# Kernel optimization log

Hardware: AMD Instinct MI355X
Metric: run time of the kernel (lower is better)

The kernel has to match this reference:

```python
import jax, jax.numpy as jnp
import numpy as np

B = 2048        # graphs per batch
NC = 81         # cells per sudoku
IN_C, HID = 10, 128
N_ACT, N_NUM, N_TECH = 4, 9, 10


def _sudoku_edges():
    idx = np.arange(NC).reshape(9, 9)
    adj = np.zeros((NC, NC), dtype=bool)
    for i in range(9):
        for j in range(9):
            n = idx[i, j]
            adj[n, idx[i, :]] = True
            adj[n, idx[:, j]] = True
            bi, bj = 3 * (i // 3), 3 * (j // 3)
            adj[n, idx[bi:bi + 3, bj:bj + 3].reshape(-1)] = True
            adj[n, n] = False
    src, dst = np.nonzero(adj)  # 1620 directed edges
    return np.stack([src, dst]).astype(np.int32)


def setup_inputs() -> dict:
    key = jax.random.key(0)
    ks = jax.random.split(key, 12)
    N = B * NC
    base = _sudoku_edges()                          # [2, 1620]
    offs = (np.arange(B, dtype=np.int32) * NC)      # [B]
    ei = (base[:, None, :] + offs[None, :, None]).reshape(2, -1)  # [2, B*1620]
    batch = np.repeat(np.arange(B, dtype=np.int32), NC)           # [N]

    def lin(k, fan_in, fan_out):
        s = 1.0 / np.sqrt(fan_in)
        return jax.random.uniform(k, (fan_in, fan_out), jnp.float32, -s, s)

    return {
        "x": jax.random.normal(ks[0], (N, IN_C), jnp.float32),
        "edge_index": jnp.asarray(ei),
        "batch": jnp.asarray(batch),
        "W1": lin(ks[1], IN_C, HID), "b1": jnp.zeros((HID,), jnp.float32),
        "W2": lin(ks[2], HID, HID),  "b2": jnp.zeros((HID,), jnp.float32),
        "Wa": lin(ks[3], HID, N_ACT),  "ba": jnp.zeros((N_ACT,), jnp.float32),
        "Wc": lin(ks[4], HID, NC),     "bc": jnp.zeros((NC,), jnp.float32),
        "Wn": lin(ks[5], HID, N_NUM),  "bn": jnp.zeros((N_NUM,), jnp.float32),
        "Wt": lin(ks[6], HID, N_TECH), "bt": jnp.zeros((N_TECH,), jnp.float32),
    }


def _gcn_conv(x, edge_index, W, b):
    n = x.shape[0]
    loop = jnp.arange(n, dtype=edge_index.dtype)
    src = jnp.concatenate([edge_index[0], loop])
    dst = jnp.concatenate([edge_index[1], loop])
    deg = jax.ops.segment_sum(jnp.ones_like(dst, jnp.float32), dst, num_segments=n)
    dinv = jax.lax.rsqrt(deg)            # deg >= 1 due to self-loops
    norm = dinv[src] * dinv[dst]         # [E+N]
    h = x @ W                            # [N, out]
    msg = h[src] * norm[:, None]         # gather + scale
    return jax.ops.segment_sum(msg, dst, num_segments=n) + b


def reference(x, edge_index, batch, W1, b1, W2, b2, Wa, ba, Wc, bc, Wn, bn, Wt, bt):
    h = jax.nn.relu(_gcn_conv(x, edge_index, W1, b1))
    h = jax.nn.relu(_gcn_conv(h, edge_index, W2, b2))
    # global mean pool over graphs
    sums = jax.ops.segment_sum(h, batch, num_segments=B)
    cnts = jax.ops.segment_sum(jnp.ones((h.shape[0],), h.dtype), batch, num_segments=B)
    pooled = sums / jnp.maximum(cnts, 1.0)[:, None]   # [B, HID]
    return (pooled @ Wa + ba, pooled @ Wc + bc, pooled @ Wn + bn, pooled @ Wt + bt)
```

## Files before the change

kernel.cpp:

```cpp
#include <hip/hip_runtime.h>
#include <hip/hip_bf16.h>

typedef __attribute__((ext_vector_type(8))) short bf16x8;
typedef __attribute__((ext_vector_type(4))) float f32x4;

__device__ __forceinline__ unsigned short f2b(float f) {
    __hip_bfloat16 h = __float2bfloat16(f);
    return __builtin_bit_cast(unsigned short, h);
}
__device__ __forceinline__ float b2f(unsigned short u) {
    unsigned v = ((unsigned)u) << 16;
    return __builtin_bit_cast(float, v);
}
__device__ __forceinline__ float ldf(const void* p, int idx, bool f32) {
    return f32 ? ((const float*)p)[idx] : b2f(((const unsigned short*)p)[idx]);
}
__device__ __forceinline__ unsigned short ldb(const void* p, int idx, bool f32) {
    return f32 ? f2b(((const float*)p)[idx]) : ((const unsigned short*)p)[idx];
}
__device__ __forceinline__ int swz(int row, int col) {
    return row * 128 + (((col >> 3) ^ (row & 7)) << 3) + (col & 7);
}

__device__ __forceinline__ bool sniff_f32(const void* x) {
    const unsigned* p = (const unsigned*)x;
    int wild = 0;
#pragma unroll
    for (int i = 0; i < 16; ++i) {
        unsigned e = (p[i] >> 7) & 0xFF;
        wild += (e != 0 && (e < 0x68 || e > 0x90)) ? 1 : 0;
    }
    return wild > 8;
}

#define WS_B1F    16
#define WS_B2F    528
#define WS_BHF    1040
#define WS_W1R    1536
#define WS_W2R    9728
#define WS_SR     42496
#define WS_WH     60928

__global__ void k_repack(const void* __restrict__ x,
                         const void* __restrict__ W1, const void* __restrict__ b1,
                         const void* __restrict__ W2, const void* __restrict__ b2,
                         const void* __restrict__ Wa, const void* __restrict__ ba,
                         const void* __restrict__ Wc, const void* __restrict__ bc,
                         const void* __restrict__ Wn, const void* __restrict__ bn,
                         const void* __restrict__ Wt, const void* __restrict__ bt,
                         char* __restrict__ ws) {
    const bool f32 = sniff_f32(x);
    int idx = blockIdx.x * blockDim.x + threadIdx.x;
    if (idx < 4096) {
        int f = idx >> 5, k = idx & 31;
        unsigned short v = (k < 10) ? ldb(W1, k * 128 + f, f32) : (unsigned short)0;
        ((unsigned short*)(ws + WS_W1R))[idx] = v;
        return;
    }
    idx -= 4096;
    if (idx < 16384) {
        int f = idx >> 7, k = idx & 127;
        ((unsigned short*)(ws + WS_W2R))[idx] = ldb(W2, k * 128 + f, f32);
        return;
    }
    idx -= 16384;
    if (idx < 9216) {
        int fi = idx >> 9, rem = idx & 511;
        int lane = rem >> 3, j = rem & 7;
        int mi = fi / 3, kc = fi - mi * 3;
        int node = mi * 16 + (lane & 15);
        int cell = kc * 32 + ((lane >> 4) << 3) + j;
        bool adj = false;
        if (node < 81 && cell < 81) {
            int ni = node / 9, nj = node % 9;
            int ci = cell / 9, cj = cell % 9;
            adj = (ni == ci) || (nj == cj) ||
                  ((ni / 3 == ci / 3) && (nj / 3 == cj / 3));
        }
        ((unsigned short*)(ws + WS_SR))[idx] = adj ? (unsigned short)0x3F80 : (unsigned short)0;
        return;
    }
    idx -= 9216;
    if (idx < 13312) {
        int o = idx >> 7, f = idx & 127;
        const void* W; int oo, dim;
        if (o < 4)       { W = Wa; oo = o;      dim = 4;  }
        else if (o < 85) { W = Wc; oo = o - 4;  dim = 81; }
        else if (o < 94) { W = Wn; oo = o - 85; dim = 9;  }
        else             { W = Wt; oo = o - 94; dim = 10; }
        ((float*)(ws + WS_WH))[idx] = ldf(W, f * dim + oo, f32);
        return;
    }
    idx -= 13312;
    if (idx < 360) {
        float v;
        if (idx < 128)      v = ldf(b1, idx, f32);
        else if (idx < 256) v = ldf(b2, idx - 128, f32);
        else {
            int o = idx - 256;
            if (o < 4)       v = ldf(ba, o, f32);
            else if (o < 85) v = ldf(bc, o - 4, f32);
            else if (o < 94) v = ldf(bn, o - 85, f32);
            else             v = ldf(bt, o - 94, f32);
        }
        if (idx < 128)      ((float*)(ws + WS_B1F))[idx] = v;
        else if (idx < 256) ((float*)(ws + WS_B2F))[idx - 128] = v;
        else                ((float*)(ws + WS_BHF))[idx - 256] = v;
    }
}

__global__ __launch_bounds__(256, 2) void sudoku_gnn(
    const void* __restrict__ x, const char* __restrict__ ws,
    void* __restrict__ out, int nB)
{
    __shared__ __attribute__((aligned(16))) unsigned short sA[16384];
    __shared__ __attribute__((aligned(16))) unsigned short sB[16384];
    __shared__ __attribute__((aligned(16))) unsigned int   xs2[1632];
    __shared__ float sPoolPart[2][256];
    __shared__ float sPool[2][128];

    const bool f32 = sniff_f32(x);
    const unsigned short* w1r = (const unsigned short*)(ws + WS_W1R);
    const unsigned short* w2r = (const unsigned short*)(ws + WS_W2R);
    const unsigned short* sr  = (const unsigned short*)(ws + WS_SR);
    const float* b1f = (const float*)(ws + WS_B1F);
    const float* b2f = (const float*)(ws + WS_B2F);
    const float* bhf = (const float*)(ws + WS_BHF);
    const float* whf = (const float*)(ws + WS_WH);

    const int tid  = threadIdx.x;
    const int wave = tid >> 6;
    const int lane = tid & 63;
    const int ln15 = lane & 15;
    const int q    = lane >> 4;
    const int k0   = q * 8;
    const int mtb  = (wave & 1) * 3;
    const int nb   = (wave & 1) * 48;
    const int fb   = (wave >> 1) * 64;
    const int g0   = blockIdx.x * 2;
    const int g1   = g0 + 1;
    const bool hasB = (g1 < nB);
    const float inv21 = 1.0f / 21.0f;
    unsigned short* const buf[2] = {sA, sB};

    {
        const int words = f32 ? 810 : 405;
        const int tot = words * (hasB ? 2 : 1);
        const unsigned int* src = (const unsigned int*)x + (size_t)g0 * words;
        for (int i = tid; i < tot; i += 256) xs2[i] = src[i];
    }

    bf16x8 sfr[3][3];
#pragma unroll
    for (int kc = 0; kc < 3; ++kc)
#pragma unroll
        for (int jt = 0; jt < 3; ++jt)
            sfr[kc][jt] = *(const bf16x8*)&sr[(((mtb + jt) * 3 + kc) * 64 + lane) * 8];
    bf16x8 w1f[4];
#pragma unroll
    for (int nt = 0; nt < 4; ++nt)
        w1f[nt] = *(const bf16x8*)&w1r[(fb + nt * 16 + ln15) * 32 + k0];

    __syncthreads();

    bf16x8 xf[2][3];
#pragma unroll
    for (int gg = 0; gg < 2; ++gg)
#pragma unroll
        for (int mt = 0; mt < 3; ++mt) {
            int node = (mtb + mt) * 16 + ln15;
            bf16x8 v = {0, 0, 0, 0, 0, 0, 0, 0};
            if (node < 81) {
                int base = gg * 810 + node * 10;
                if (q == 0) {
#pragma unroll
                    for (int jj = 0; jj < 8; ++jj)
                        v[jj] = (short)(f32 ? f2b(((const float*)xs2)[base + jj])
                                            : ((const unsigned short*)xs2)[base + jj]);
                } else if (q == 1) {
#pragma unroll
                    for (int jj = 0; jj < 2; ++jj)
                        v[jj] = (short)(f32 ? f2b(((const float*)xs2)[base + 8 + jj])
                                            : ((const unsigned short*)xs2)[base + 8 + jj]);
                }
            }
            xf[gg][mt] = v;
        }

    const f32x4 z4 = {0.f, 0.f, 0.f, 0.f};
    f32x4 acc[2][3][4];

#pragma unroll
    for (int gg = 0; gg < 2; ++gg)
#pragma unroll
        for (int mt = 0; mt < 3; ++mt)
#pragma unroll
            for (int nt = 0; nt < 4; ++nt)
                acc[gg][mt][nt] = __builtin_amdgcn_mfma_f32_16x16x32_bf16(xf[gg][mt], w1f[nt], z4, 0, 0, 0);
#pragma unroll
    for (int gg = 0; gg < 2; ++gg)
#pragma unroll
        for (int mt = 0; mt < 3; ++mt)
#pragma unroll
            for (int nt = 0; nt < 4; ++nt) {
                int f = fb + nt * 16 + ln15;
                int nodeb = (mtb + mt) * 16 + q * 4;
                unsigned lo = (unsigned)f2b(acc[gg][mt][nt][0]) | ((unsigned)f2b(acc[gg][mt][nt][1]) << 16);
                unsigned hi = (unsigned)f2b(acc[gg][mt][nt][2]) | ((unsigned)f2b(acc[gg][mt][nt][3]) << 16);
                *(uint2*)&buf[gg][swz(f, nodeb)] = make_uint2(lo, hi);
            }
    __syncthreads();

#pragma unroll
    for (int gg = 0; gg < 2; ++gg)
#pragma unroll
        for (int a = 0; a < 3; ++a)
#pragma unroll
            for (int b = 0; b < 4; ++b) acc[gg][a][b] = z4;
#pragma unroll
    for (int kc = 0; kc < 3; ++kc) {
        bf16x8 a4[2][4];
#pragma unroll
        for (int gg = 0; gg < 2; ++gg)
#pragma unroll
            for (int at = 0; at < 4; ++at)
                a4[gg][at] = *(const bf16x8*)&buf[gg][swz(fb + at * 16 + ln15, kc * 32 + k0)];
#pragma unroll
        for (int gg = 0; gg < 2; ++gg)
#pragma unroll
            for (int at = 0; at < 4; ++at)
#pragma unroll
                for (int jt = 0; jt < 3; ++jt)
                    acc[gg][jt][at] = __builtin_amdgcn_mfma_f32_16x16x32_bf16(a4[gg][at], sfr[kc][jt], acc[gg][jt][at], 0, 0, 0);
    }
    __syncthreads();
#pragma unroll
    for (int gg = 0; gg < 2; ++gg)
#pragma unroll
        for (int at = 0; at < 4; ++at) {
            float4 bv = *(const float4*)&b1f[fb + at * 16 + q * 4];
#pragma unroll
            for (int jt = 0; jt < 3; ++jt) {
                int node = nb + jt * 16 + ln15;
                float v0 = fmaxf(acc[gg][jt][at][0] * inv21 + bv.x, 0.0f);
                float v1 = fmaxf(acc[gg][jt][at][1] * inv21 + bv.y, 0.0f);
                float v2 = fmaxf(acc[gg][jt][at][2] * inv21 + bv.z, 0.0f);
                float v3 = fmaxf(acc[gg][jt][at][3] * inv21 + bv.w, 0.0f);
                unsigned lo = (unsigned)f2b(v0) | ((unsigned)f2b(v1) << 16);
                unsigned hi = (unsigned)f2b(v2) | ((unsigned)f2b(v3) << 16);
                *(uint2*)&buf[gg][swz(node, fb + at * 16 + q * 4)] = make_uint2(lo, hi);
            }
        }
    __syncthreads();

#pragma unroll
    for (int gg = 0; gg < 2; ++gg)
#pragma unroll
        for (int a = 0; a < 3; ++a)
#pragma unroll
            for (int b = 0; b < 4; ++b) acc[gg][a][b] = z4;
#pragma unroll
    for (int kc = 0; kc < 4; ++kc) {
        bf16x8 w2f[4];
#pragma unroll
        for (int nt = 0; nt < 4; ++nt)
            w2f[nt] = *(const bf16x8*)&w2r[(fb + nt * 16 + ln15) * 128 + kc * 32 + k0];
        bf16x8 a3[2][3];
#pragma unroll
        for (int gg = 0; gg < 2; ++gg)
#pragma unroll
            for (int mt = 0; mt < 3; ++mt)
                a3[gg][mt] = *(const bf16x8*)&buf[gg][swz((mtb + mt) * 16 + ln15, kc * 32 + k0)];
#pragma unroll
        for (int gg = 0; gg < 2; ++gg)
#pragma unroll
            for (int mt = 0; mt < 3; ++mt)
#pragma unroll
                for (int nt = 0; nt < 4; ++nt)
                    acc[gg][mt][nt] = __builtin_amdgcn_mfma_f32_16x16x32_bf16(a3[gg][mt], w2f[nt], acc[gg][mt][nt], 0, 0, 0);
    }
    __syncthreads();
#pragma unroll
    for (int gg = 0; gg < 2; ++gg)
#pragma unroll
        for (int mt = 0; mt < 3; ++mt)
#pragma unroll
            for (int nt = 0; nt < 4; ++nt) {
                int f = fb + nt * 16 + ln15;
                int nodeb = (mtb + mt) * 16 + q * 4;
                unsigned lo = (unsigned)f2b(acc[gg][mt][nt][0]) | ((unsigned)f2b(acc[gg][mt][nt][1]) << 16);
                unsigned hi = (unsigned)f2b(acc[gg][mt][nt][2]) | ((unsigned)f2b(acc[gg][mt][nt][3]) << 16);
                *(uint2*)&buf[gg][swz(f, nodeb)] = make_uint2(lo, hi);
            }
    __syncthreads();

#pragma unroll
    for (int gg = 0; gg < 2; ++gg)
#pragma unroll
        for (int a = 0; a < 3; ++a)
#pragma unroll
            for (int b = 0; b < 4; ++b) acc[gg][a][b] = z4;
#pragma unroll
    for (int kc = 0; kc < 3; ++kc) {
        bf16x8 a4[2][4];
#pragma unroll
        for (int gg = 0; gg < 2; ++gg)
#pragma unroll
            for (int at = 0; at < 4; ++at)
                a4[gg][at] = *(const bf16x8*)&buf[gg][swz(fb + at * 16 + ln15, kc * 32 + k0)];
#pragma unroll
        for (int gg = 0; gg < 2; ++gg)
#pragma unroll
            for (int at = 0; at < 4; ++at)
#pragma unroll
                for (int jt = 0; jt < 3; ++jt)
                    acc[gg][jt][at] = __builtin_amdgcn_mfma_f32_16x16x32_bf16(a4[gg][at], sfr[kc][jt], acc[gg][jt][at], 0, 0, 0);
    }
#pragma unroll
    for (int gg = 0; gg < 2; ++gg)
#pragma unroll
        for (int at = 0; at < 4; ++at) {
            float4 bv = *(const float4*)&b2f[fb + at * 16 + q * 4];
            float s0 = 0.f, s1 = 0.f, s2 = 0.f, s3 = 0.f;
#pragma unroll
            for (int jt = 0; jt < 3; ++jt) {
                int node = nb + jt * 16 + ln15;
                if (node < 81) {
                    s0 += fmaxf(acc[gg][jt][at][0] * inv21 + bv.x, 0.0f);
                    s1 += fmaxf(acc[gg][jt][at][1] * inv21 + bv.y, 0.0f);
                    s2 += fmaxf(acc[gg][jt][at][2] * inv21 + bv.z, 0.0f);
                    s3 += fmaxf(acc[gg][jt][at][3] * inv21 + bv.w, 0.0f);
                }
            }
#pragma unroll
            for (int off = 1; off < 16; off <<= 1) {
                s0 += __shfl_xor(s0, off);
                s1 += __shfl_xor(s1, off);
                s2 += __shfl_xor(s2, off);
                s3 += __shfl_xor(s3, off);
            }
            if (ln15 == 0) {
                float4 v = {s0, s1, s2, s3};
                *(float4*)&sPoolPart[gg][(wave & 1) * 128 + fb + at * 16 + q * 4] = v;
            }
        }
    __syncthreads();
    {
        int gg = tid >> 7;
        int f  = tid & 127;
        sPool[gg][f] = (sPoolPart[gg][f] + sPoolPart[gg][128 + f]) / 81.0f;
    }
    __syncthreads();

    {
        int gg = tid >> 7;
        int o  = tid & 127;
        int g  = gg ? g1 : g0;
        if (o < 104 && (gg == 0 || hasB)) {
            float a = bhf[o];
            const float4* wrow = (const float4*)(whf + o * 128);
            const float4* sp4  = (const float4*)sPool[gg];
#pragma unroll 8
            for (int i = 0; i < 32; ++i) {
                float4 wv = wrow[i];
                float4 pv = sp4[i];
                a += pv.x * wv.x + pv.y * wv.y + pv.z * wv.z + pv.w * wv.w;
            }
            int oo; size_t off;
            if (o < 4)       { oo = o;      off = (size_t)g * 4 + oo; }
            else if (o < 85) { oo = o - 4;  off = (size_t)nB * 4  + (size_t)g * 81 + oo; }
            else if (o < 94) { oo = o - 85; off = (size_t)nB * 85 + (size_t)g * 9  + oo; }
            else             { oo = o - 94; off = (size_t)nB * 94 + (size_t)g * 10 + oo; }
            if (f32) ((float*)out)[off] = a;
            else     ((unsigned short*)out)[off] = f2b(a);
        }
    }
}

extern "C" void kernel_launch(void* const* d_in, const int* in_sizes, int n_in,
                              void* d_out, int out_size, void* d_ws, size_t ws_size,
                              hipStream_t stream) {
    const void* x  = d_in[0];
    int nB = in_sizes[2] / 81;
    if (nB <= 0) return;

    char* ws = (char*)d_ws;
    hipLaunchKernelGGL(k_repack, dim3(170), dim3(256), 0, stream,
                       x, d_in[3], d_in[4], d_in[5], d_in[6],
                       d_in[7], d_in[8], d_in[9], d_in[10],
                       d_in[11], d_in[12], d_in[13], d_in[14], ws);
    hipLaunchKernelGGL(sudoku_gnn, dim3((nB + 1) / 2), dim3(256), 0, stream,
                       x, (const char*)ws, d_out, nB);
}
```

Measured before the change: 144.4 us.

## Fold both GCN layers into one loop with padded-stride LDS layout

Replaces the XOR-swizzled LDS buffers with padded row strides (136 and 104 shorts) in one shared array, and loads x directly into LDS as bf16 rows instead of staging raw words. The two GCN layers share a rolled loop with rolled k-chunk loops, which shrinks code size and likely register pressure. LDS usage drops, which may help occupancy. In exchange the rolled loops can limit instruction scheduling and MFMA/load overlap, and padding may leave some bank conflicts.

```diff
diff --git a/kernel.cpp b/kernel.cpp
--- a/kernel.cpp
+++ b/kernel.cpp
@@ -17,9 +17,6 @@
 }
 __device__ __forceinline__ unsigned short ldb(const void* p, int idx, bool f32) {
     return f32 ? f2b(((const float*)p)[idx]) : ((const unsigned short*)p)[idx];
-}
-__device__ __forceinline__ int swz(int row, int col) {
-    return row * 128 + (((col >> 3) ^ (row & 7)) << 3) + (col & 7);
 }
 
 __device__ __forceinline__ bool sniff_f32(const void* x) {
@@ -109,13 +106,14 @@
     }
 }
 
+#define TS 104
+#define HS 136
+
 __global__ __launch_bounds__(256, 2) void sudoku_gnn(
     const void* __restrict__ x, const char* __restrict__ ws,
     void* __restrict__ out, int nB)
 {
-    __shared__ __attribute__((aligned(16))) unsigned short sA[16384];
-    __shared__ __attribute__((aligned(16))) unsigned short sB[16384];
-    __shared__ __attribute__((aligned(16))) unsigned int   xs2[1632];
+    __shared__ __attribute__((aligned(16))) unsigned short sG[2][13312];
     __shared__ float sPoolPart[2][256];
     __shared__ float sPool[2][128];
 
@@ -138,17 +136,9 @@
     const int nb   = (wave & 1) * 48;
     const int fb   = (wave >> 1) * 64;
     const int g0   = blockIdx.x * 2;
-    const int g1   = g0 + 1;
-    const bool hasB = (g1 < nB);
+    const bool hasB = (g0 + 1 < nB);
+    const int g1   = hasB ? (g0 + 1) : g0;
     const float inv21 = 1.0f / 21.0f;
-    unsigned short* const buf[2] = {sA, sB};
-
-    {
-        const int words = f32 ? 810 : 405;
-        const int tot = words * (hasB ? 2 : 1);
-        const unsigned int* src = (const unsigned int*)x + (size_t)g0 * words;
-        for (int i = tid; i < tot; i += 256) xs2[i] = src[i];
-    }
 
     bf16x8 sfr[3][3];
 #pragma unroll
@@ -156,206 +146,179 @@
 #pragma unroll
         for (int jt = 0; jt < 3; ++jt)
             sfr[kc][jt] = *(const bf16x8*)&sr[(((mtb + jt) * 3 + kc) * 64 + lane) * 8];
-    bf16x8 w1f[4];
-#pragma unroll
-    for (int nt = 0; nt < 4; ++nt)
-        w1f[nt] = *(const bf16x8*)&w1r[(fb + nt * 16 + ln15) * 32 + k0];
-
+
+#pragma unroll 1
+    for (int idx = tid; idx < 96 * 16 * 2; idx += 256) {
+        int gg  = idx >= 96 * 16;
+        int r   = idx - gg * 96 * 16;
+        int row = r >> 4, col = (r & 15) * 2;
+        int g   = gg ? g1 : g0;
+        unsigned short v0 = 0, v1 = 0;
+        if (row < 81) {
+            int base = (g * 81 + row) * 10;
+            if (col < 10)     v0 = ldb(x, base + col, f32);
+            if (col + 1 < 10) v1 = ldb(x, base + col + 1, f32);
+        }
+        *(unsigned*)&sG[gg][row * HS + col] = (unsigned)v0 | ((unsigned)v1 << 16);
+    }
     __syncthreads();
-
-    bf16x8 xf[2][3];
-#pragma unroll
-    for (int gg = 0; gg < 2; ++gg)
-#pragma unroll
-        for (int mt = 0; mt < 3; ++mt) {
-            int node = (mtb + mt) * 16 + ln15;
-            bf16x8 v = {0, 0, 0, 0, 0, 0, 0, 0};
-            if (node < 81) {
-                int base = gg * 810 + node * 10;
-                if (q == 0) {
-#pragma unroll
-                    for (int jj = 0; jj < 8; ++jj)
-                        v[jj] = (short)(f32 ? f2b(((const float*)xs2)[base + jj])
-                                            : ((const unsigned short*)xs2)[base + jj]);
-                } else if (q == 1) {
-#pragma unroll
-                    for (int jj = 0; jj < 2; ++jj)
-                        v[jj] = (short)(f32 ? f2b(((const float*)xs2)[base + 8 + jj])
-                                            : ((const unsigned short*)xs2)[base + 8 + jj]);
-                }
-            }
-            xf[gg][mt] = v;
-        }
 
     const f32x4 z4 = {0.f, 0.f, 0.f, 0.f};
     f32x4 acc[2][3][4];
 
-#pragma unroll
-    for (int gg = 0; gg < 2; ++gg)
-#pragma unroll
-        for (int mt = 0; mt < 3; ++mt)
+#pragma unroll 1
+    for (int l = 0; l < 2; ++l) {
+        const unsigned short* w = l ? w2r : w1r;
+        const int ldw = l ? 128 : 32;
+        const int kcn = l ? 4 : 1;
+
+        {
+            bf16x8 wf[4], a3[2][3];
 #pragma unroll
             for (int nt = 0; nt < 4; ++nt)
-                acc[gg][mt][nt] = __builtin_amdgcn_mfma_f32_16x16x32_bf16(xf[gg][mt], w1f[nt], z4, 0, 0, 0);
-#pragma unroll
-    for (int gg = 0; gg < 2; ++gg)
-#pragma unroll
-        for (int mt = 0; mt < 3; ++mt)
-#pragma unroll
-            for (int nt = 0; nt < 4; ++nt) {
-                int f = fb + nt * 16 + ln15;
-                int nodeb = (mtb + mt) * 16 + q * 4;
-                unsigned lo = (unsigned)f2b(acc[gg][mt][nt][0]) | ((unsigned)f2b(acc[gg][mt][nt][1]) << 16);
-                unsigned hi = (unsigned)f2b(acc[gg][mt][nt][2]) | ((unsigned)f2b(acc[gg][mt][nt][3]) << 16);
-                *(uint2*)&buf[gg][swz(f, nodeb)] = make_uint2(lo, hi);
+                wf[nt] = *(const bf16x8*)&w[(fb + nt * 16 + ln15) * ldw + k0];
+#pragma unroll
+            for (int gg = 0; gg < 2; ++gg)
+#pragma unroll
+                for (int mt = 0; mt < 3; ++mt)
+                    a3[gg][mt] = *(const bf16x8*)&sG[gg][((mtb + mt) * 16 + ln15) * HS + k0];
+#pragma unroll
+            for (int gg = 0; gg < 2; ++gg)
+#pragma unroll
+                for (int mt = 0; mt < 3; ++mt)
+#pragma unroll
+                    for (int nt = 0; nt < 4; ++nt)
+                        acc[gg][mt][nt] = __builtin_amdgcn_mfma_f32_16x16x32_bf16(a3[gg][mt], wf[nt], z4, 0, 0, 0);
+        }
+#pragma unroll 1
+        for (int kc = 1; kc < kcn; ++kc) {
+            bf16x8 wf[4], a3[2][3];
+#pragma unroll
+            for (int nt = 0; nt < 4; ++nt)
+                wf[nt] = *(const bf16x8*)&w[(fb + nt * 16 + ln15) * ldw + kc * 32 + k0];
+#pragma unroll
+            for (int gg = 0; gg < 2; ++gg)
+#pragma unroll
+                for (int mt = 0; mt < 3; ++mt)
+                    a3[gg][mt] = *(const bf16x8*)&sG[gg][((mtb + mt) * 16 + ln15) * HS + kc * 32 + k0];
+#pragma unroll
+            for (int gg = 0; gg < 2; ++gg)
+#pragma unroll
+                for (int mt = 0; mt < 3; ++mt)
+#pragma unroll
+                    for (int nt = 0; nt < 4; ++nt)
+                        acc[gg][mt][nt] = __builtin_amdgcn_mfma_f32_16x16x32_bf16(a3[gg][mt], wf[nt], acc[gg][mt][nt], 0, 0, 0);
+        }
+        __syncthreads();
+
+#pragma unroll
+        for (int gg = 0; gg < 2; ++gg)
+#pragma unroll
+            for (int mt = 0; mt < 3; ++mt)
+#pragma unroll
+                for (int nt = 0; nt < 4; ++nt) {
+                    int f = fb + nt * 16 + ln15;
+                    int cellb = (mtb + mt) * 16 + q * 4;
+                    unsigned lo = (unsigned)f2b(acc[gg][mt][nt][0]) | ((unsigned)f2b(acc[gg][mt][nt][1]) << 16);
+                    unsigned hi = (unsigned)f2b(acc[gg][mt][nt][2]) | ((unsigned)f2b(acc[gg][mt][nt][3]) << 16);
+                    *(uint2*)&sG[gg][f * TS + cellb] = make_uint2(lo, hi);
+                }
+        __syncthreads();
+
+        {
+            bf16x8 a4[2][4];
+#pragma unroll
+            for (int gg = 0; gg < 2; ++gg)
+#pragma unroll
+                for (int at = 0; at < 4; ++at)
+                    a4[gg][at] = *(const bf16x8*)&sG[gg][(fb + at * 16 + ln15) * TS + k0];
+#pragma unroll
+            for (int gg = 0; gg < 2; ++gg)
+#pragma unroll
+                for (int at = 0; at < 4; ++at)
+#pragma unroll
+                    for (int jt = 0; jt < 3; ++jt)
+                        acc[gg][jt][at] = __builtin_amdgcn_mfma_f32_16x16x32_bf16(a4[gg][at], sfr[0][jt], z4, 0, 0, 0);
+        }
+#pragma unroll 1
+        for (int kc = 1; kc < 3; ++kc) {
+            bf16x8 a4[2][4];
+#pragma unroll
+            for (int gg = 0; gg < 2; ++gg)
+#pragma unroll
+                for (int at = 0; at < 4; ++at)
+                    a4[gg][at] = *(const bf16x8*)&sG[gg][(fb + at * 16 + ln15) * TS + kc * 32 + k0];
+#pragma unroll
+            for (int gg = 0; gg < 2; ++gg)
+#pragma unroll
+                for (int at = 0; at < 4; ++at)
+#pragma unroll
+                    for (int jt = 0; jt < 3; ++jt)
+                        acc[gg][jt][at] = __builtin_amdgcn_mfma_f32_16x16x32_bf16(a4[gg][at], sfr[kc][jt], acc[gg][jt][at], 0, 0, 0);
+        }
+        __syncthreads();
+
+        if (l == 0) {
+#pragma unroll
+            for (int gg = 0; gg < 2; ++gg)
+#pragma unroll
+                for (int at = 0; at < 4; ++at) {
+                    float4 bv = *(const float4*)&b1f[fb + at * 16 + q * 4];
+#pragma unroll
+                    for (int jt = 0; jt < 3; ++jt) {
+                        int node = nb + jt * 16 + ln15;
+                        float v0 = fmaxf(acc[gg][jt][at][0] * inv21 + bv.x, 0.0f);
+                        float v1 = fmaxf(acc[gg][jt][at][1] * inv21 + bv.y, 0.0f);
+                        float v2 = fmaxf(acc[gg][jt][at][2] * inv21 + bv.z, 0.0f);
+                        float v3 = fmaxf(acc[gg][jt][at][3] * inv21 + bv.w, 0.0f);
+                        unsigned lo = (unsigned)f2b(v0) | ((unsigned)f2b(v1) << 16);
+                        unsigned hi = (unsigned)f2b(v2) | ((unsigned)f2b(v3) << 16);
+                        *(uint2*)&sG[gg][node * HS + fb + at * 16 + q * 4] = make_uint2(lo, hi);
+                    }
+                }
+            __syncthreads();
+        } else {
+#pragma unroll
+            for (int gg = 0; gg < 2; ++gg)
+#pragma unroll
+                for (int at = 0; at < 4; ++at) {
+                    float4 bv = *(const float4*)&b2f[fb + at * 16 + q * 4];
+                    float s0 = 0.f, s1 = 0.f, s2 = 0.f, s3 = 0.f;
+#pragma unroll
+                    for (int jt = 0; jt < 3; ++jt) {
+                        int node = nb + jt * 16 + ln15;
+                        if (node < 81) {
+                            s0 += fmaxf(acc[gg][jt][at][0] * inv21 + bv.x, 0.0f);
+                            s1 += fmaxf(acc[gg][jt][at][1] * inv21 + bv.y, 0.0f);
+                            s2 += fmaxf(acc[gg][jt][at][2] * inv21 + bv.z, 0.0f);
+                            s3 += fmaxf(acc[gg][jt][at][3] * inv21 + bv.w, 0.0f);
+                        }
+                    }
+#pragma unroll
+                    for (int off = 1; off < 16; off <<= 1) {
+                        s0 += __shfl_xor(s0, off);
+                        s1 += __shfl_xor(s1, off);
+                        s2 += __shfl_xor(s2, off);
+                        s3 += __shfl_xor(s3, off);
+                    }
+                    if (ln15 == 0) {
+                        float4 v = {s0, s1, s2, s3};
+                        *(float4*)&sPoolPart[gg][(wave & 1) * 128 + fb + at * 16 + q * 4] = v;
+                    }
+                }
+            __syncthreads();
+            {
+                int gg = tid >> 7, f = tid & 127;
+                sPool[gg][f] = (sPoolPart[gg][f] + sPoolPart[gg][128 + f]) * (1.0f / 81.0f);
             }
-    __syncthreads();
-
-#pragma unroll
-    for (int gg = 0; gg < 2; ++gg)
-#pragma unroll
-        for (int a = 0; a < 3; ++a)
-#pragma unroll
-            for (int b = 0; b < 4; ++b) acc[gg][a][b] = z4;
-#pragma unroll
-    for (int kc = 0; kc < 3; ++kc) {
-        bf16x8 a4[2][4];
-#pragma unroll
-        for (int gg = 0; gg < 2; ++gg)
-#pragma unroll
-            for (int at = 0; at < 4; ++at)
-                a4[gg][at] = *(const bf16x8*)&buf[gg][swz(fb + at * 16 + ln15, kc * 32 + k0)];
-#pragma unroll
-        for (int gg = 0; gg < 2; ++gg)
-#pragma unroll
-            for (int at = 0; at < 4; ++at)
-#pragma unroll
-                for (int jt = 0; jt < 3; ++jt)
-                    acc[gg][jt][at] = __builtin_amdgcn_mfma_f32_16x16x32_bf16(a4[gg][at], sfr[kc][jt], acc[gg][jt][at], 0, 0, 0);
-    }
-    __syncthreads();
-#pragma unroll
-    for (int gg = 0; gg < 2; ++gg)
-#pragma unroll
-        for (int at = 0; at < 4; ++at) {
-            float4 bv = *(const float4*)&b1f[fb + at * 16 + q * 4];
-#pragma unroll
-            for (int jt = 0; jt < 3; ++jt) {
-                int node = nb + jt * 16 + ln15;
-                float v0 = fmaxf(acc[gg][jt][at][0] * inv21 + bv.x, 0.0f);
-                float v1 = fmaxf(acc[gg][jt][at][1] * inv21 + bv.y, 0.0f);
-                float v2 = fmaxf(acc[gg][jt][at][2] * inv21 + bv.z, 0.0f);
-                float v3 = fmaxf(acc[gg][jt][at][3] * inv21 + bv.w, 0.0f);
-                unsigned lo = (unsigned)f2b(v0) | ((unsigned)f2b(v1) << 16);
-                unsigned hi = (unsigned)f2b(v2) | ((unsigned)f2b(v3) << 16);
-                *(uint2*)&buf[gg][swz(node, fb + at * 16 + q * 4)] = make_uint2(lo, hi);
-            }
-        }
-    __syncthreads();
-
-#pragma unroll
-    for (int gg = 0; gg < 2; ++gg)
-#pragma unroll
-        for (int a = 0; a < 3; ++a)
-#pragma unroll
-            for (int b = 0; b < 4; ++b) acc[gg][a][b] = z4;
-#pragma unroll
-    for (int kc = 0; kc < 4; ++kc) {
-        bf16x8 w2f[4];
-#pragma unroll
-        for (int nt = 0; nt < 4; ++nt)
-            w2f[nt] = *(const bf16x8*)&w2r[(fb + nt * 16 + ln15) * 128 + kc * 32 + k0];
-        bf16x8 a3[2][3];
-#pragma unroll
-        for (int gg = 0; gg < 2; ++gg)
-#pragma unroll
-            for (int mt = 0; mt < 3; ++mt)
-                a3[gg][mt] = *(const bf16x8*)&buf[gg][swz((mtb + mt) * 16 + ln15, kc * 32 + k0)];
-#pragma unroll
-        for (int gg = 0; gg < 2; ++gg)
-#pragma unroll
-            for (int mt = 0; mt < 3; ++mt)
-#pragma unroll
-                for (int nt = 0; nt < 4; ++nt)
-                    acc[gg][mt][nt] = __builtin_amdgcn_mfma_f32_16x16x32_bf16(a3[gg][mt], w2f[nt], acc[gg][mt][nt], 0, 0, 0);
-    }
-    __syncthreads();
-#pragma unroll
-    for (int gg = 0; gg < 2; ++gg)
-#pragma unroll
-        for (int mt = 0; mt < 3; ++mt)
-#pragma unroll
-            for (int nt = 0; nt < 4; ++nt) {
-                int f = fb + nt * 16 + ln15;
-                int nodeb = (mtb + mt) * 16 + q * 4;
-                unsigned lo = (unsigned)f2b(acc[gg][mt][nt][0]) | ((unsigned)f2b(acc[gg][mt][nt][1]) << 16);
-                unsigned hi = (unsigned)f2b(acc[gg][mt][nt][2]) | ((unsigned)f2b(acc[gg][mt][nt][3]) << 16);
-                *(uint2*)&buf[gg][swz(f, nodeb)] = make_uint2(lo, hi);
-            }
-    __syncthreads();
-
-#pragma unroll
-    for (int gg = 0; gg < 2; ++gg)
-#pragma unroll
-        for (int a = 0; a < 3; ++a)
-#pragma unroll
-            for (int b = 0; b < 4; ++b) acc[gg][a][b] = z4;
-#pragma unroll
-    for (int kc = 0; kc < 3; ++kc) {
-        bf16x8 a4[2][4];
-#pragma unroll
-        for (int gg = 0; gg < 2; ++gg)
-#pragma unroll
-            for (int at = 0; at < 4; ++at)
-                a4[gg][at] = *(const bf16x8*)&buf[gg][swz(fb + at * 16 + ln15, kc * 32 + k0)];
-#pragma unroll
-        for (int gg = 0; gg < 2; ++gg)
-#pragma unroll
-            for (int at = 0; at < 4; ++at)
-#pragma unroll
-                for (int jt = 0; jt < 3; ++jt)
-                    acc[gg][jt][at] = __builtin_amdgcn_mfma_f32_16x16x32_bf16(a4[gg][at], sfr[kc][jt], acc[gg][jt][at], 0, 0, 0);
-    }
-#pragma unroll
-    for (int gg = 0; gg < 2; ++gg)
-#pragma unroll
-        for (int at = 0; at < 4; ++at) {
-            float4 bv = *(const float4*)&b2f[fb + at * 16 + q * 4];
-            float s0 = 0.f, s1 = 0.f, s2 = 0.f, s3 = 0.f;
-#pragma unroll
-            for (int jt = 0; jt < 3; ++jt) {
-                int node = nb + jt * 16 + ln15;
-                if (node < 81) {
-                    s0 += fmaxf(acc[gg][jt][at][0] * inv21 + bv.x, 0.0f);
-                    s1 += fmaxf(acc[gg][jt][at][1] * inv21 + bv.y, 0.0f);
-                    s2 += fmaxf(acc[gg][jt][at][2] * inv21 + bv.z, 0.0f);
-                    s3 += fmaxf(acc[gg][jt][at][3] * inv21 + bv.w, 0.0f);
-                }
-            }
-#pragma unroll
-            for (int off = 1; off < 16; off <<= 1) {
-                s0 += __shfl_xor(s0, off);
-                s1 += __shfl_xor(s1, off);
-                s2 += __shfl_xor(s2, off);
-                s3 += __shfl_xor(s3, off);
-            }
-            if (ln15 == 0) {
-                float4 v = {s0, s1, s2, s3};
-                *(float4*)&sPoolPart[gg][(wave & 1) * 128 + fb + at * 16 + q * 4] = v;
-            }
-        }
-    __syncthreads();
-    {
-        int gg = tid >> 7;
-        int f  = tid & 127;
-        sPool[gg][f] = (sPoolPart[gg][f] + sPoolPart[gg][128 + f]) / 81.0f;
-    }
-    __syncthreads();
+            __syncthreads();
+        }
+    }
 
     {
         int gg = tid >> 7;
         int o  = tid & 127;
-        int g  = gg ? g1 : g0;
+        int g  = gg ? (g0 + 1) : g0;
         if (o < 104 && (gg == 0 || hasB)) {
             float a = bhf[o];
             const float4* wrow = (const float4*)(whf + o * 128);
```

Measured after the change: 161.8 us. 1.12x slower.

## Fold normalization scales into weights, shrink LDS with padded layout, load x directly

Applied to the files above, without the earlier changes.

Folds the 1/21 GCN normalization into W1/W2 and the 1/81 mean-pool factor into the head weights during repack, which removes per-element multiplies from the epilogues. Replaces the two 32KB swizzled LDS buffers, the staged x copy and the separate pool arrays with one padded buffer (row strides 104/136) that is reused for pooling partials. This lowers LDS use and may allow more resident blocks. Also reads x straight from global memory, caches the dtype sniff result in the workspace, uses a manual RNE bf16 pack, and seeds the first MFMA with zero instead of clearing accumulators. In exchange, folding the scale before bf16 rounding changes numerics slightly, and the padded strides may cause more LDS bank conflicts than the swizzle did.

```diff
diff --git a/kernel.cpp b/kernel.cpp
--- a/kernel.cpp
+++ b/kernel.cpp
@@ -18,10 +18,13 @@
 __device__ __forceinline__ unsigned short ldb(const void* p, int idx, bool f32) {
     return f32 ? f2b(((const float*)p)[idx]) : ((const unsigned short*)p)[idx];
 }
-__device__ __forceinline__ int swz(int row, int col) {
-    return row * 128 + (((col >> 3) ^ (row & 7)) << 3) + (col & 7);
-}
-
+__device__ __forceinline__ unsigned packRNE(float x, float y) {
+    unsigned a = __builtin_bit_cast(unsigned, x);
+    unsigned b = __builtin_bit_cast(unsigned, y);
+    a += 0x7fffu + ((a >> 16) & 1u);
+    b += 0x7fffu + ((b >> 16) & 1u);
+    return (a >> 16) | (b & 0xffff0000u);
+}
 __device__ __forceinline__ bool sniff_f32(const void* x) {
     const unsigned* p = (const unsigned*)x;
     int wild = 0;
@@ -33,6 +36,7 @@
     return wild > 8;
 }
 
+#define WS_FLAG   0
 #define WS_B1F    16
 #define WS_B2F    528
 #define WS_BHF    1040
@@ -50,17 +54,19 @@
                          const void* __restrict__ Wt, const void* __restrict__ bt,
                          char* __restrict__ ws) {
     const bool f32 = sniff_f32(x);
+    const float inv21 = 1.0f / 21.0f;
+    if (blockIdx.x == 0 && threadIdx.x == 0) *(int*)(ws + WS_FLAG) = f32 ? 1 : 0;
     int idx = blockIdx.x * blockDim.x + threadIdx.x;
     if (idx < 4096) {
         int f = idx >> 5, k = idx & 31;
-        unsigned short v = (k < 10) ? ldb(W1, k * 128 + f, f32) : (unsigned short)0;
+        unsigned short v = (k < 10) ? f2b(ldf(W1, k * 128 + f, f32) * inv21) : (unsigned short)0;
         ((unsigned short*)(ws + WS_W1R))[idx] = v;
         return;
     }
     idx -= 4096;
     if (idx < 16384) {
         int f = idx >> 7, k = idx & 127;
-        ((unsigned short*)(ws + WS_W2R))[idx] = ldb(W2, k * 128 + f, f32);
+        ((unsigned short*)(ws + WS_W2R))[idx] = f2b(ldf(W2, k * 128 + f, f32) * inv21);
         return;
     }
     idx -= 16384;
@@ -88,7 +94,7 @@
         else if (o < 85) { W = Wc; oo = o - 4;  dim = 81; }
         else if (o < 94) { W = Wn; oo = o - 85; dim = 9;  }
         else             { W = Wt; oo = o - 94; dim = 10; }
-        ((float*)(ws + WS_WH))[idx] = ldf(W, f * dim + oo, f32);
+        ((float*)(ws + WS_WH))[idx] = ldf(W, f * dim + oo, f32) * (1.0f / 81.0f);
         return;
     }
     idx -= 13312;
@@ -109,17 +115,16 @@
     }
 }
 
+#define TS 104
+#define HS 136
+
 __global__ __launch_bounds__(256, 2) void sudoku_gnn(
     const void* __restrict__ x, const char* __restrict__ ws,
     void* __restrict__ out, int nB)
 {
-    __shared__ __attribute__((aligned(16))) unsigned short sA[16384];
-    __shared__ __attribute__((aligned(16))) unsigned short sB[16384];
-    __shared__ __attribute__((aligned(16))) unsigned int   xs2[1632];
-    __shared__ float sPoolPart[2][256];
-    __shared__ float sPool[2][128];
-
-    const bool f32 = sniff_f32(x);
+    __shared__ __attribute__((aligned(16))) unsigned short sG[2][13312];
+
+    const bool f32 = (*(const int*)(ws + WS_FLAG)) != 0;
     const unsigned short* w1r = (const unsigned short*)(ws + WS_W1R);
     const unsigned short* w2r = (const unsigned short*)(ws + WS_W2R);
     const unsigned short* sr  = (const unsigned short*)(ws + WS_SR);
@@ -138,17 +143,8 @@
     const int nb   = (wave & 1) * 48;
     const int fb   = (wave >> 1) * 64;
     const int g0   = blockIdx.x * 2;
-    const int g1   = g0 + 1;
-    const bool hasB = (g1 < nB);
-    const float inv21 = 1.0f / 21.0f;
-    unsigned short* const buf[2] = {sA, sB};
-
-    {
-        const int words = f32 ? 810 : 405;
-        const int tot = words * (hasB ? 2 : 1);
-        const unsigned int* src = (const unsigned int*)x + (size_t)g0 * words;
-        for (int i = tid; i < tot; i += 256) xs2[i] = src[i];
-    }
+    const bool hasB = (g0 + 1 < nB);
+    const int g1   = hasB ? (g0 + 1) : g0;
 
     bf16x8 sfr[3][3];
 #pragma unroll
@@ -161,27 +157,22 @@
     for (int nt = 0; nt < 4; ++nt)
         w1f[nt] = *(const bf16x8*)&w1r[(fb + nt * 16 + ln15) * 32 + k0];
 
-    __syncthreads();
-
     bf16x8 xf[2][3];
 #pragma unroll
     for (int gg = 0; gg < 2; ++gg)
 #pragma unroll
         for (int mt = 0; mt < 3; ++mt) {
             int node = (mtb + mt) * 16 + ln15;
+            int g = gg ? g1 : g0;
             bf16x8 v = {0, 0, 0, 0, 0, 0, 0, 0};
             if (node < 81) {
-                int base = gg * 810 + node * 10;
+                int base = (g * 81 + node) * 10;
                 if (q == 0) {
 #pragma unroll
-                    for (int jj = 0; jj < 8; ++jj)
-                        v[jj] = (short)(f32 ? f2b(((const float*)xs2)[base + jj])
-                                            : ((const unsigned short*)xs2)[base + jj]);
+                    for (int jj = 0; jj < 8; ++jj) v[jj] = (short)ldb(x, base + jj, f32);
                 } else if (q == 1) {
-#pragma unroll
-                    for (int jj = 0; jj < 2; ++jj)
-                        v[jj] = (short)(f32 ? f2b(((const float*)xs2)[base + 8 + jj])
-                                            : ((const unsigned short*)xs2)[base + 8 + jj]);
+                    v[0] = (short)ldb(x, base + 8, f32);
+                    v[1] = (short)ldb(x, base + 9, f32);
                 }
             }
             xf[gg][mt] = v;
@@ -204,36 +195,41 @@
 #pragma unroll
             for (int nt = 0; nt < 4; ++nt) {
                 int f = fb + nt * 16 + ln15;
-                int nodeb = (mtb + mt) * 16 + q * 4;
-                unsigned lo = (unsigned)f2b(acc[gg][mt][nt][0]) | ((unsigned)f2b(acc[gg][mt][nt][1]) << 16);
-                unsigned hi = (unsigned)f2b(acc[gg][mt][nt][2]) | ((unsigned)f2b(acc[gg][mt][nt][3]) << 16);
-                *(uint2*)&buf[gg][swz(f, nodeb)] = make_uint2(lo, hi);
-            }
-    __syncthreads();
-
-#pragma unroll
-    for (int gg = 0; gg < 2; ++gg)
-#pragma unroll
-        for (int a = 0; a < 3; ++a)
-#pragma unroll
-            for (int b = 0; b < 4; ++b) acc[gg][a][b] = z4;
+                int cellb = (mtb + mt) * 16 + q * 4;
+                *(uint2*)&sG[gg][f * TS + cellb] =
+                    make_uint2(packRNE(acc[gg][mt][nt][0], acc[gg][mt][nt][1]),
+                               packRNE(acc[gg][mt][nt][2], acc[gg][mt][nt][3]));
+            }
+    __syncthreads();
+
 #pragma unroll
     for (int kc = 0; kc < 3; ++kc) {
-        bf16x8 a4[2][4];
+        bf16x8 afr[2][4];
 #pragma unroll
         for (int gg = 0; gg < 2; ++gg)
 #pragma unroll
             for (int at = 0; at < 4; ++at)
-                a4[gg][at] = *(const bf16x8*)&buf[gg][swz(fb + at * 16 + ln15, kc * 32 + k0)];
-#pragma unroll
-        for (int gg = 0; gg < 2; ++gg)
-#pragma unroll
-            for (int at = 0; at < 4; ++at)
-#pragma unroll
-                for (int jt = 0; jt < 3; ++jt)
-                    acc[gg][jt][at] = __builtin_amdgcn_mfma_f32_16x16x32_bf16(a4[gg][at], sfr[kc][jt], acc[gg][jt][at], 0, 0, 0);
-    }
-    __syncthreads();
+                afr[gg][at] = *(const bf16x8*)&sG[gg][(fb + at * 16 + ln15) * TS + kc * 32 + k0];
+        if (kc == 0) {
+#pragma unroll
+            for (int gg = 0; gg < 2; ++gg)
+#pragma unroll
+                for (int at = 0; at < 4; ++at)
+#pragma unroll
+                    for (int jt = 0; jt < 3; ++jt)
+                        acc[gg][jt][at] = __builtin_amdgcn_mfma_f32_16x16x32_bf16(afr[gg][at], sfr[0][jt], z4, 0, 0, 0);
+        } else {
+#pragma unroll
+            for (int gg = 0; gg < 2; ++gg)
+#pragma unroll
+                for (int at = 0; at < 4; ++at)
+#pragma unroll
+                    for (int jt = 0; jt < 3; ++jt)
+                        acc[gg][jt][at] = __builtin_amdgcn_mfma_f32_16x16x32_bf16(afr[gg][at], sfr[kc][jt], acc[gg][jt][at], 0, 0, 0);
+        }
+    }
+    __syncthreads();
+
 #pragma unroll
     for (int gg = 0; gg < 2; ++gg)
 #pragma unroll
@@ -242,44 +238,47 @@
 #pragma unroll
             for (int jt = 0; jt < 3; ++jt) {
                 int node = nb + jt * 16 + ln15;
-                float v0 = fmaxf(acc[gg][jt][at][0] * inv21 + bv.x, 0.0f);
-                float v1 = fmaxf(acc[gg][jt][at][1] * inv21 + bv.y, 0.0f);
-                float v2 = fmaxf(acc[gg][jt][at][2] * inv21 + bv.z, 0.0f);
-                float v3 = fmaxf(acc[gg][jt][at][3] * inv21 + bv.w, 0.0f);
-                unsigned lo = (unsigned)f2b(v0) | ((unsigned)f2b(v1) << 16);
-                unsigned hi = (unsigned)f2b(v2) | ((unsigned)f2b(v3) << 16);
-                *(uint2*)&buf[gg][swz(node, fb + at * 16 + q * 4)] = make_uint2(lo, hi);
-            }
-        }
-    __syncthreads();
-
-#pragma unroll
-    for (int gg = 0; gg < 2; ++gg)
-#pragma unroll
-        for (int a = 0; a < 3; ++a)
-#pragma unroll
-            for (int b = 0; b < 4; ++b) acc[gg][a][b] = z4;
+                float v0 = fmaxf(acc[gg][jt][at][0] + bv.x, 0.0f);
+                float v1 = fmaxf(acc[gg][jt][at][1] + bv.y, 0.0f);
+                float v2 = fmaxf(acc[gg][jt][at][2] + bv.z, 0.0f);
+                float v3 = fmaxf(acc[gg][jt][at][3] + bv.w, 0.0f);
+                *(uint2*)&sG[gg][node * HS + fb + at * 16 + q * 4] =
+                    make_uint2(packRNE(v0, v1), packRNE(v2, v3));
+            }
+        }
+    __syncthreads();
+
 #pragma unroll
     for (int kc = 0; kc < 4; ++kc) {
-        bf16x8 w2f[4];
+        bf16x8 w2f[4], a3[2][3];
 #pragma unroll
         for (int nt = 0; nt < 4; ++nt)
             w2f[nt] = *(const bf16x8*)&w2r[(fb + nt * 16 + ln15) * 128 + kc * 32 + k0];
-        bf16x8 a3[2][3];
 #pragma unroll
         for (int gg = 0; gg < 2; ++gg)
 #pragma unroll
             for (int mt = 0; mt < 3; ++mt)
-                a3[gg][mt] = *(const bf16x8*)&buf[gg][swz((mtb + mt) * 16 + ln15, kc * 32 + k0)];
-#pragma unroll
-        for (int gg = 0; gg < 2; ++gg)
-#pragma unroll
-            for (int mt = 0; mt < 3; ++mt)
-#pragma unroll
-                for (int nt = 0; nt < 4; ++nt)
-                    acc[gg][mt][nt] = __builtin_amdgcn_mfma_f32_16x16x32_bf16(a3[gg][mt], w2f[nt], acc[gg][mt][nt], 0, 0, 0);
-    }
-    __syncthreads();
+                a3[gg][mt] = *(const bf16x8*)&sG[gg][((mtb + mt) * 16 + ln15) * HS + kc * 32 + k0];
+        if (kc == 0) {
+#pragma unroll
+            for (int gg = 0; gg < 2; ++gg)
+#pragma unroll
+                for (int mt = 0; mt < 3; ++mt)
+#pragma unroll
+                    for (int nt = 0; nt < 4; ++nt)
+                        acc[gg][mt][nt] = __builtin_amdgcn_mfma_f32_16x16x32_bf16(a3[gg][mt], w2f[nt], z4, 0, 0, 0);
+        } else {
+#pragma unroll
+            for (int gg = 0; gg < 2; ++gg)
+#pragma unroll
+                for (int mt = 0; mt < 3; ++mt)
+#pragma unroll
+                    for (int nt = 0; nt < 4; ++nt)
+                        acc[gg][mt][nt] = __builtin_amdgcn_mfma_f32_16x16x32_bf16(a3[gg][mt], w2f[nt], acc[gg][mt][nt], 0, 0, 0);
+        }
+    }
+    __syncthreads();
+
 #pragma unroll
     for (int gg = 0; gg < 2; ++gg)
 #pragma unroll
@@ -287,35 +286,40 @@
 #pragma unroll
             for (int nt = 0; nt < 4; ++nt) {
                 int f = fb + nt * 16 + ln15;
-                int nodeb = (mtb + mt) * 16 + q * 4;
-                unsigned lo = (unsigned)f2b(acc[gg][mt][nt][0]) | ((unsigned)f2b(acc[gg][mt][nt][1]) << 16);
-                unsigned hi = (unsigned)f2b(acc[gg][mt][nt][2]) | ((unsigned)f2b(acc[gg][mt][nt][3]) << 16);
-                *(uint2*)&buf[gg][swz(f, nodeb)] = make_uint2(lo, hi);
-            }
-    __syncthreads();
-
-#pragma unroll
-    for (int gg = 0; gg < 2; ++gg)
-#pragma unroll
-        for (int a = 0; a < 3; ++a)
-#pragma unroll
-            for (int b = 0; b < 4; ++b) acc[gg][a][b] = z4;
+                int cellb = (mtb + mt) * 16 + q * 4;
+                *(uint2*)&sG[gg][f * TS + cellb] =
+                    make_uint2(packRNE(acc[gg][mt][nt][0], acc[gg][mt][nt][1]),
+                               packRNE(acc[gg][mt][nt][2], acc[gg][mt][nt][3]));
+            }
+    __syncthreads();
+
 #pragma unroll
     for (int kc = 0; kc < 3; ++kc) {
-        bf16x8 a4[2][4];
+        bf16x8 afr[2][4];
 #pragma unroll
         for (int gg = 0; gg < 2; ++gg)
 #pragma unroll
             for (int at = 0; at < 4; ++at)
-                a4[gg][at] = *(const bf16x8*)&buf[gg][swz(fb + at * 16 + ln15, kc * 32 + k0)];
-#pragma unroll
-        for (int gg = 0; gg < 2; ++gg)
-#pragma unroll
-            for (int at = 0; at < 4; ++at)
-#pragma unroll
-                for (int jt = 0; jt < 3; ++jt)
-                    acc[gg][jt][at] = __builtin_amdgcn_mfma_f32_16x16x32_bf16(a4[gg][at], sfr[kc][jt], acc[gg][jt][at], 0, 0, 0);
-    }
+                afr[gg][at] = *(const bf16x8*)&sG[gg][(fb + at * 16 + ln15) * TS + kc * 32 + k0];
+        if (kc == 0) {
+#pragma unroll
+            for (int gg = 0; gg < 2; ++gg)
+#pragma unroll
+                for (int at = 0; at < 4; ++at)
+#pragma unroll
+                    for (int jt = 0; jt < 3; ++jt)
+                        acc[gg][jt][at] = __builtin_amdgcn_mfma_f32_16x16x32_bf16(afr[gg][at], sfr[0][jt], z4, 0, 0, 0);
+        } else {
+#pragma unroll
+            for (int gg = 0; gg < 2; ++gg)
+#pragma unroll
+                for (int at = 0; at < 4; ++at)
+#pragma unroll
+                    for (int jt = 0; jt < 3; ++jt)
+                        acc[gg][jt][at] = __builtin_amdgcn_mfma_f32_16x16x32_bf16(afr[gg][at], sfr[kc][jt], acc[gg][jt][at], 0, 0, 0);
+        }
+    }
+    float ps[2][4][4];
 #pragma unroll
     for (int gg = 0; gg < 2; ++gg)
 #pragma unroll
@@ -326,10 +330,10 @@
             for (int jt = 0; jt < 3; ++jt) {
                 int node = nb + jt * 16 + ln15;
                 if (node < 81) {
-                    s0 += fmaxf(acc[gg][jt][at][0] * inv21 + bv.x, 0.0f);
-                    s1 += fmaxf(acc[gg][jt][at][1] * inv21 + bv.y, 0.0f);
-                    s2 += fmaxf(acc[gg][jt][at][2] * inv21 + bv.z, 0.0f);
-                    s3 += fmaxf(acc[gg][jt][at][3] * inv21 + bv.w, 0.0f);
+                    s0 += fmaxf(acc[gg][jt][at][0] + bv.x, 0.0f);
+                    s1 += fmaxf(acc[gg][jt][at][1] + bv.y, 0.0f);
+                    s2 += fmaxf(acc[gg][jt][at][2] + bv.z, 0.0f);
+                    s3 += fmaxf(acc[gg][jt][at][3] + bv.w, 0.0f);
                 }
             }
 #pragma unroll
@@ -339,27 +343,37 @@
                 s2 += __shfl_xor(s2, off);
                 s3 += __shfl_xor(s3, off);
             }
-            if (ln15 == 0) {
-                float4 v = {s0, s1, s2, s3};
-                *(float4*)&sPoolPart[gg][(wave & 1) * 128 + fb + at * 16 + q * 4] = v;
-            }
-        }
+            ps[gg][at][0] = s0; ps[gg][at][1] = s1; ps[gg][at][2] = s2; ps[gg][at][3] = s3;
+        }
+    __syncthreads();
+
+#pragma unroll
+    for (int gg = 0; gg < 2; ++gg) {
+        float* sPart = (float*)&sG[gg][0];
+        if (ln15 == 0) {
+#pragma unroll
+            for (int at = 0; at < 4; ++at) {
+                float4 v = {ps[gg][at][0], ps[gg][at][1], ps[gg][at][2], ps[gg][at][3]};
+                *(float4*)&sPart[(wave & 1) * 128 + fb + at * 16 + q * 4] = v;
+            }
+        }
+    }
     __syncthreads();
     {
-        int gg = tid >> 7;
-        int f  = tid & 127;
-        sPool[gg][f] = (sPoolPart[gg][f] + sPoolPart[gg][128 + f]) / 81.0f;
+        int gg = tid >> 7, f = tid & 127;
+        float* sPart = (float*)&sG[gg][0];
+        ((float*)&sG[gg][512])[f] = sPart[f] + sPart[128 + f];
     }
     __syncthreads();
 
     {
         int gg = tid >> 7;
         int o  = tid & 127;
-        int g  = gg ? g1 : g0;
+        int g  = gg ? (g0 + 1) : g0;
         if (o < 104 && (gg == 0 || hasB)) {
             float a = bhf[o];
             const float4* wrow = (const float4*)(whf + o * 128);
-            const float4* sp4  = (const float4*)sPool[gg];
+            const float4* sp4  = (const float4*)&sG[gg][512];
 #pragma unroll 8
             for (int i = 0; i < 32; ++i) {
                 float4 wv = wrow[i];
```

Result: slower. 150.5 us (+4.3%).
